# Kernel tuning notes

Hardware: AMD Instinct MI355X
Metric: run time of the kernel (lower is better)

The kernel has to match this reference:

```python
import jax, jax.numpy as jnp
import numpy as np

H = 8
SPLIT = 1
# deterministic stand-in for random.shuffle(range(8)) in the original
_PERM = np.random.RandomState(0).permutation(H)
SERIES_IDX = jnp.asarray(_PERM[SPLIT:])  # 7 heads
CROSS_IDX = jnp.asarray(_PERM[:SPLIT])   # 1 head


def setup_inputs() -> dict:
    key = jax.random.key(0)
    ks = jax.random.split(key, 5)
    B, L, E = 8, 1024, 64
    shp = (B, L, H, E)
    return {
        "queries": jax.random.normal(ks[0], shp, dtype=jnp.float32),
        "keys": jax.random.normal(ks[1], shp, dtype=jnp.float32),
        "keysT": jax.random.normal(ks[2], shp, dtype=jnp.float32),
        "values": jax.random.normal(ks[3], shp, dtype=jnp.float32),
        "valuesT": jax.random.normal(ks[4], shp, dtype=jnp.float32),
    }


def reference(queries, keys, keysT, values, valuesT):
    B, L, _, E = queries.shape
    scale = 1.0 / jnp.sqrt(jnp.asarray(E, dtype=queries.dtype))
    neg_inf = jnp.asarray(-jnp.inf, dtype=queries.dtype)

    # head split (gather along head dim)
    sq = queries[:, :, SERIES_IDX]   # [B,L,7,E]
    sk = keys[:, :, SERIES_IDX]      # [B,S,7,E]
    sv = values[:, :, SERIES_IDX]    # [B,S,7,D]
    cq = queries[:, :, CROSS_IDX]    # [B,L,1,E]
    ckT = keysT[:, :, CROSS_IDX]     # [B,C,1,E]
    cvT = valuesT[:, :, CROSS_IDX]   # [B,C,1,D]

    # causal mask: True above the diagonal -> disallowed
    causal = jnp.triu(jnp.ones((L, L), dtype=bool), k=1)  # [L,L]

    # series branch
    scores = jnp.einsum('blne,bsne->bnls', sq, sk)  # [B,7,L,S]
    scores = jnp.where(causal[None, None], neg_inf, scores * scale)
    series = jax.nn.softmax(scores, axis=-1)
    V = jnp.einsum('bhls,bshd->blhd', series, sv)   # [B,L,7,D]

    # cross branch
    cscores = jnp.einsum('blme,bcme->bmlc', cq, ckT)  # [B,1,L,C]
    cscores = jnp.where(causal[None, None], neg_inf, cscores * scale)
    crosses = jax.nn.softmax(cscores, axis=-1)
    V_cross = jnp.einsum('bhlc,bchd->blhd', crosses, cvT)  # [B,L,1,D]

    return jnp.concatenate([V, V_cross], axis=2)  # [B,L,8,D]
```

## Files before the change

kernel.cpp:

```cpp
#include <hip/hip_runtime.h>
#include <math.h>

#define Lq 1024
#define Hq 8
#define Eq 64
#define LDW 72

#define SRC_HEAD_PACKED 0x64503712u

typedef __bf16 bf16_t;
typedef __bf16 bf16x8 __attribute__((ext_vector_type(8)));
typedef __bf16 bf16x4 __attribute__((ext_vector_type(4)));
typedef float floatx4 __attribute__((ext_vector_type(4)));

__device__ __forceinline__ bf16x8 cvt8(const float4 a, const float4 b) {
    bf16x8 r;
    r[0] = (bf16_t)a.x; r[1] = (bf16_t)a.y; r[2] = (bf16_t)a.z; r[3] = (bf16_t)a.w;
    r[4] = (bf16_t)b.x; r[5] = (bf16_t)b.y; r[6] = (bf16_t)b.z; r[7] = (bf16_t)b.w;
    return r;
}

__global__ __launch_bounds__(256, 2)
void attn_mfma(const float* __restrict__ Q, const float* __restrict__ Ks,
               const float* __restrict__ KTs, const float* __restrict__ Vs,
               const float* __restrict__ VTs, float* __restrict__ out) {
    const int p    = blockIdx.x;
    const int slot = blockIdx.y;
    const int b    = blockIdx.z;
    const int h    = (SRC_HEAD_PACKED >> (slot * 4)) & 0xF;
    const float* __restrict__ Kp = (slot == 7) ? KTs : Ks;
    const float* __restrict__ Vp = (slot == 7) ? VTs : Vs;
    const int pA = p, pB = 15 - p;

    const int tid  = threadIdx.x;
    const int wv   = tid >> 6;
    const int lane = tid & 63;
    const int ln16 = lane & 15;
    const int quad = lane >> 4;

    __shared__ alignas(16) unsigned short k_lds[64][LDW];
    __shared__ alignas(16) unsigned short vt_lds[64][LDW];
    __shared__ alignas(16) unsigned short pt_lds[4][16][LDW];

    const float qs = 0.125f * 1.44269504f;
    bf16x8 qfA[2], qfB[2];
    {
        const int rA = pA * 64 + wv * 16 + ln16;
        const int rB = pB * 64 + wv * 16 + ln16;
        const float* qa = Q + (((size_t)b * Lq + rA) * Hq + h) * Eq + quad * 8;
        const float* qb = Q + (((size_t)b * Lq + rB) * Hq + h) * Eq + quad * 8;
        #pragma unroll
        for (int ec = 0; ec < 2; ++ec) {
            float4 f0 = ((const float4*)(qa + ec * 32))[0];
            float4 f1 = ((const float4*)(qa + ec * 32))[1];
            float4 g0 = ((const float4*)(qb + ec * 32))[0];
            float4 g1 = ((const float4*)(qb + ec * 32))[1];
            f0.x*=qs; f0.y*=qs; f0.z*=qs; f0.w*=qs; f1.x*=qs; f1.y*=qs; f1.z*=qs; f1.w*=qs;
            g0.x*=qs; g0.y*=qs; g0.z*=qs; g0.w*=qs; g1.x*=qs; g1.y*=qs; g1.z*=qs; g1.w*=qs;
            qfA[ec] = cvt8(f0, f1);
            qfB[ec] = cvt8(g0, g1);
        }
    }

    floatx4 OA[4], OB[4];
    #pragma unroll
    for (int i = 0; i < 4; ++i) { OA[i] = (floatx4){0,0,0,0}; OB[i] = (floatx4){0,0,0,0}; }
    float mA = -INFINITY, lA = 0.f, mB = -INFINITY, lB = 0.f;

    float4 kq[4];
    float  vq[16];
    const int kj = tid >> 2, kc = (tid & 3) * 16;
    const int vd = tid & 63, vk = (tid >> 6) * 16;

    auto load_tile = [&](int kt) {
        const float* kb = Kp + (((size_t)b * Lq + kt * 64 + kj) * Hq + h) * Eq + kc;
        kq[0] = ((const float4*)kb)[0]; kq[1] = ((const float4*)kb)[1];
        kq[2] = ((const float4*)kb)[2]; kq[3] = ((const float4*)kb)[3];
        const float* vb = Vp + (((size_t)b * Lq + kt * 64 + vk) * Hq + h) * Eq + vd;
        #pragma unroll
        for (int i = 0; i < 16; ++i) vq[i] = vb[(size_t)i * (Hq * Eq)];
    };

    auto process = [&](const bf16x8* qf, bf16x8 kf[4][2], bf16x8 vf[4][2],
                       floatx4* O, float& m, float& l, bool diag) {
        floatx4 s[4];
        #pragma unroll
        for (int nc = 0; nc < 4; ++nc) {
            floatx4 acc = (floatx4){0,0,0,0};
            acc = __builtin_amdgcn_mfma_f32_16x16x32_bf16(kf[nc][0], qf[0], acc, 0, 0, 0);
            acc = __builtin_amdgcn_mfma_f32_16x16x32_bf16(kf[nc][1], qf[1], acc, 0, 0, 0);
            s[nc] = acc;
        }
        if (diag) {
            const int rin = wv * 16 + ln16;
            #pragma unroll
            for (int nc = 0; nc < 4; ++nc)
                #pragma unroll
                for (int r = 0; r < 4; ++r)
                    if (nc * 16 + quad * 4 + r > rin) s[nc][r] = -INFINITY;
        }
        float mn = s[0][0];
        #pragma unroll
        for (int nc = 0; nc < 4; ++nc)
            #pragma unroll
            for (int r = 0; r < 4; ++r) mn = fmaxf(mn, s[nc][r]);
        mn = fmaxf(mn, __shfl_xor(mn, 16, 64));
        mn = fmaxf(mn, __shfl_xor(mn, 32, 64));
        mn = fmaxf(mn, m);
        const float alpha = __builtin_amdgcn_exp2f(m - mn);
        m = mn;
        float ps = 0.f;
        float pv[4][4];
        #pragma unroll
        for (int nc = 0; nc < 4; ++nc)
            #pragma unroll
            for (int r = 0; r < 4; ++r) { pv[nc][r] = __builtin_amdgcn_exp2f(s[nc][r] - mn); ps += pv[nc][r]; }
        ps += __shfl_xor(ps, 16, 64);
        ps += __shfl_xor(ps, 32, 64);
        l = l * alpha + ps;
        #pragma unroll
        for (int dc = 0; dc < 4; ++dc) O[dc] *= alpha;
        #pragma unroll
        for (int nc = 0; nc < 4; ++nc) {
            bf16x4 pk;
            pk[0] = (bf16_t)pv[nc][0]; pk[1] = (bf16_t)pv[nc][1];
            pk[2] = (bf16_t)pv[nc][2]; pk[3] = (bf16_t)pv[nc][3];
            *(bf16x4*)&pt_lds[wv][ln16][nc * 16 + quad * 4] = pk;
        }
        bf16x8 pf0 = *(const bf16x8*)&pt_lds[wv][ln16][quad * 8];
        bf16x8 pf1 = *(const bf16x8*)&pt_lds[wv][ln16][32 + quad * 8];
        #pragma unroll
        for (int dc = 0; dc < 4; ++dc) {
            O[dc] = __builtin_amdgcn_mfma_f32_16x16x32_bf16(vf[dc][0], pf0, O[dc], 0, 0, 0);
            O[dc] = __builtin_amdgcn_mfma_f32_16x16x32_bf16(vf[dc][1], pf1, O[dc], 0, 0, 0);
        }
    };

    load_tile(0);
    for (int kt = 0; kt <= pB; ++kt) {
        __syncthreads();
        *(bf16x8*)&k_lds[kj][kc]      = cvt8(kq[0], kq[1]);
        *(bf16x8*)&k_lds[kj][kc + 8]  = cvt8(kq[2], kq[3]);
        {
            const float4* vq4 = (const float4*)vq;
            *(bf16x8*)&vt_lds[vd][vk]     = cvt8(vq4[0], vq4[1]);
            *(bf16x8*)&vt_lds[vd][vk + 8] = cvt8(vq4[2], vq4[3]);
        }
        if (kt < pB) load_tile(kt + 1);
        __syncthreads();

        bf16x8 kf[4][2], vf[4][2];
        #pragma unroll
        for (int c = 0; c < 4; ++c) {
            kf[c][0] = *(const bf16x8*)&k_lds[c * 16 + ln16][quad * 8];
            kf[c][1] = *(const bf16x8*)&k_lds[c * 16 + ln16][32 + quad * 8];
            vf[c][0] = *(const bf16x8*)&vt_lds[c * 16 + ln16][quad * 8];
            vf[c][1] = *(const bf16x8*)&vt_lds[c * 16 + ln16][32 + quad * 8];
        }
        if (kt <= pA) process(qfA, kf, vf, OA, mA, lA, kt == pA);
        process(qfB, kf, vf, OB, mB, lB, kt == pB);
    }

    {
        const float inv = 1.0f / lA;
        const int row = pA * 64 + wv * 16 + ln16;
        float* op = out + (((size_t)b * Lq + row) * Hq + slot) * Eq + quad * 4;
        #pragma unroll
        for (int dc = 0; dc < 4; ++dc) {
            float4 o; o.x = OA[dc][0] * inv; o.y = OA[dc][1] * inv;
            o.z = OA[dc][2] * inv; o.w = OA[dc][3] * inv;
            *(float4*)(op + dc * 16) = o;
        }
    }
    {
        const float inv = 1.0f / lB;
        const int row = pB * 64 + wv * 16 + ln16;
        float* op = out + (((size_t)b * Lq + row) * Hq + slot) * Eq + quad * 4;
        #pragma unroll
        for (int dc = 0; dc < 4; ++dc) {
            float4 o; o.x = OB[dc][0] * inv; o.y = OB[dc][1] * inv;
            o.z = OB[dc][2] * inv; o.w = OB[dc][3] * inv;
            *(float4*)(op + dc * 16) = o;
        }
    }
}

extern "C" void kernel_launch(void* const* d_in, const int* in_sizes, int n_in,
                              void* d_out, int out_size, void* d_ws, size_t ws_size,
                              hipStream_t stream) {
    const float* queries = (const float*)d_in[0];
    const float* keys    = (const float*)d_in[1];
    const float* keysT   = (const float*)d_in[2];
    const float* values  = (const float*)d_in[3];
    const float* valuesT = (const float*)d_in[4];
    float* out = (float*)d_out;

    dim3 grid(8, Hq, 8);
    dim3 block(256);
    attn_mfma<<<grid, block, 0, stream>>>(queries, keys, keysT, values, valuesT, out);
}
```

Before: 143.9 us.

## Split each key tile across two wave groups with final softmax merge

Doubles the block to 512 threads (8 waves): each set of 4 waves handles half of each 64-key tile, keeping separate online-softmax states that are merged through shared memory at the end. This halves the per-wave MFMA and softmax work per tile, giving more waves to hide latency on a grid of only 512 blocks. The grid order is also changed so slot and batch vary fastest. In exchange it adds the LDS merge with extra barriers and more register and LDS pressure per block. Initial max is set to a finite value so a fully masked half does not produce NaN.

```diff
diff --git a/kernel.cpp b/kernel.cpp
--- a/kernel.cpp
+++ b/kernel.cpp
@@ -5,6 +5,7 @@
 #define Hq 8
 #define Eq 64
 #define LDW 72
+#define PTW 40
 
 #define SRC_HEAD_PACKED 0x64503712u
 
@@ -20,13 +21,13 @@
     return r;
 }
 
-__global__ __launch_bounds__(256, 2)
+__global__ __launch_bounds__(512, 4)
 void attn_mfma(const float* __restrict__ Q, const float* __restrict__ Ks,
                const float* __restrict__ KTs, const float* __restrict__ Vs,
                const float* __restrict__ VTs, float* __restrict__ out) {
-    const int p    = blockIdx.x;
-    const int slot = blockIdx.y;
-    const int b    = blockIdx.z;
+    const int slot = blockIdx.x;
+    const int b    = blockIdx.y;
+    const int p    = blockIdx.z;
     const int h    = (SRC_HEAD_PACKED >> (slot * 4)) & 0xF;
     const float* __restrict__ Kp = (slot == 7) ? KTs : Ks;
     const float* __restrict__ Vp = (slot == 7) ? VTs : Vs;
@@ -37,16 +38,19 @@
     const int lane = tid & 63;
     const int ln16 = lane & 15;
     const int quad = lane >> 4;
-
-    __shared__ alignas(16) unsigned short k_lds[64][LDW];
-    __shared__ alignas(16) unsigned short vt_lds[64][LDW];
-    __shared__ alignas(16) unsigned short pt_lds[4][16][LDW];
+    const int wq   = wv & 3;
+    const int kh   = wv >> 2;
+
+    __shared__ alignas(16) unsigned short smem[64 * LDW * 2 + 8 * 16 * PTW];
+    unsigned short (*k_lds)[LDW]  = (unsigned short (*)[LDW])smem;
+    unsigned short (*vt_lds)[LDW] = (unsigned short (*)[LDW])(smem + 64 * LDW);
+    unsigned short (*pt)[PTW]     = (unsigned short (*)[PTW])(smem + 2 * 64 * LDW + wv * 16 * PTW);
 
     const float qs = 0.125f * 1.44269504f;
     bf16x8 qfA[2], qfB[2];
     {
-        const int rA = pA * 64 + wv * 16 + ln16;
-        const int rB = pB * 64 + wv * 16 + ln16;
+        const int rA = pA * 64 + wq * 16 + ln16;
+        const int rB = pB * 64 + wq * 16 + ln16;
         const float* qa = Q + (((size_t)b * Lq + rA) * Hq + h) * Eq + quad * 8;
         const float* qb = Q + (((size_t)b * Lq + rB) * Hq + h) * Eq + quad * 8;
         #pragma unroll
@@ -65,43 +69,42 @@
     floatx4 OA[4], OB[4];
     #pragma unroll
     for (int i = 0; i < 4; ++i) { OA[i] = (floatx4){0,0,0,0}; OB[i] = (floatx4){0,0,0,0}; }
-    float mA = -INFINITY, lA = 0.f, mB = -INFINITY, lB = 0.f;
-
-    float4 kq[4];
-    float  vq[16];
-    const int kj = tid >> 2, kc = (tid & 3) * 16;
-    const int vd = tid & 63, vk = (tid >> 6) * 16;
+    float mA = -1e30f, lA = 0.f, mB = -1e30f, lB = 0.f;
+
+    float4 kq[2];
+    float  vq[8];
+    const int kj = tid >> 3, kc = (tid & 7) * 8;
+    const int vd = tid & 63, vk = wv * 8;
 
     auto load_tile = [&](int kt) {
         const float* kb = Kp + (((size_t)b * Lq + kt * 64 + kj) * Hq + h) * Eq + kc;
         kq[0] = ((const float4*)kb)[0]; kq[1] = ((const float4*)kb)[1];
-        kq[2] = ((const float4*)kb)[2]; kq[3] = ((const float4*)kb)[3];
         const float* vb = Vp + (((size_t)b * Lq + kt * 64 + vk) * Hq + h) * Eq + vd;
         #pragma unroll
-        for (int i = 0; i < 16; ++i) vq[i] = vb[(size_t)i * (Hq * Eq)];
+        for (int i = 0; i < 8; ++i) vq[i] = vb[(size_t)i * (Hq * Eq)];
     };
 
-    auto process = [&](const bf16x8* qf, bf16x8 kf[4][2], bf16x8 vf[4][2],
+    auto process = [&](const bf16x8* qf, const bf16x8 kf[2][2], const bf16x8 vf[4],
                        floatx4* O, float& m, float& l, bool diag) {
-        floatx4 s[4];
-        #pragma unroll
-        for (int nc = 0; nc < 4; ++nc) {
+        floatx4 s[2];
+        #pragma unroll
+        for (int nc = 0; nc < 2; ++nc) {
             floatx4 acc = (floatx4){0,0,0,0};
             acc = __builtin_amdgcn_mfma_f32_16x16x32_bf16(kf[nc][0], qf[0], acc, 0, 0, 0);
             acc = __builtin_amdgcn_mfma_f32_16x16x32_bf16(kf[nc][1], qf[1], acc, 0, 0, 0);
             s[nc] = acc;
         }
         if (diag) {
-            const int rin = wv * 16 + ln16;
+            const int rin = wq * 16 + ln16;
             #pragma unroll
-            for (int nc = 0; nc < 4; ++nc)
+            for (int nc = 0; nc < 2; ++nc)
                 #pragma unroll
                 for (int r = 0; r < 4; ++r)
-                    if (nc * 16 + quad * 4 + r > rin) s[nc][r] = -INFINITY;
+                    if (kh * 32 + nc * 16 + quad * 4 + r > rin) s[nc][r] = -INFINITY;
         }
         float mn = s[0][0];
         #pragma unroll
-        for (int nc = 0; nc < 4; ++nc)
+        for (int nc = 0; nc < 2; ++nc)
             #pragma unroll
             for (int r = 0; r < 4; ++r) mn = fmaxf(mn, s[nc][r]);
         mn = fmaxf(mn, __shfl_xor(mn, 16, 64));
@@ -110,9 +113,9 @@
         const float alpha = __builtin_amdgcn_exp2f(m - mn);
         m = mn;
         float ps = 0.f;
-        float pv[4][4];
-        #pragma unroll
-        for (int nc = 0; nc < 4; ++nc)
+        float pv[2][4];
+        #pragma unroll
+        for (int nc = 0; nc < 2; ++nc)
             #pragma unroll
             for (int r = 0; r < 4; ++r) { pv[nc][r] = __builtin_amdgcn_exp2f(s[nc][r] - mn); ps += pv[nc][r]; }
         ps += __shfl_xor(ps, 16, 64);
@@ -121,65 +124,103 @@
         #pragma unroll
         for (int dc = 0; dc < 4; ++dc) O[dc] *= alpha;
         #pragma unroll
-        for (int nc = 0; nc < 4; ++nc) {
+        for (int nc = 0; nc < 2; ++nc) {
             bf16x4 pk;
             pk[0] = (bf16_t)pv[nc][0]; pk[1] = (bf16_t)pv[nc][1];
             pk[2] = (bf16_t)pv[nc][2]; pk[3] = (bf16_t)pv[nc][3];
-            *(bf16x4*)&pt_lds[wv][ln16][nc * 16 + quad * 4] = pk;
-        }
-        bf16x8 pf0 = *(const bf16x8*)&pt_lds[wv][ln16][quad * 8];
-        bf16x8 pf1 = *(const bf16x8*)&pt_lds[wv][ln16][32 + quad * 8];
-        #pragma unroll
-        for (int dc = 0; dc < 4; ++dc) {
-            O[dc] = __builtin_amdgcn_mfma_f32_16x16x32_bf16(vf[dc][0], pf0, O[dc], 0, 0, 0);
-            O[dc] = __builtin_amdgcn_mfma_f32_16x16x32_bf16(vf[dc][1], pf1, O[dc], 0, 0, 0);
-        }
+            *(bf16x4*)&pt[ln16][nc * 16 + quad * 4] = pk;
+        }
+        bf16x8 pf = *(const bf16x8*)&pt[ln16][quad * 8];
+        #pragma unroll
+        for (int dc = 0; dc < 4; ++dc)
+            O[dc] = __builtin_amdgcn_mfma_f32_16x16x32_bf16(vf[dc], pf, O[dc], 0, 0, 0);
     };
 
     load_tile(0);
     for (int kt = 0; kt <= pB; ++kt) {
         __syncthreads();
-        *(bf16x8*)&k_lds[kj][kc]      = cvt8(kq[0], kq[1]);
-        *(bf16x8*)&k_lds[kj][kc + 8]  = cvt8(kq[2], kq[3]);
+        *(bf16x8*)&k_lds[kj][kc] = cvt8(kq[0], kq[1]);
         {
             const float4* vq4 = (const float4*)vq;
-            *(bf16x8*)&vt_lds[vd][vk]     = cvt8(vq4[0], vq4[1]);
-            *(bf16x8*)&vt_lds[vd][vk + 8] = cvt8(vq4[2], vq4[3]);
+            *(bf16x8*)&vt_lds[vd][vk] = cvt8(vq4[0], vq4[1]);
         }
         if (kt < pB) load_tile(kt + 1);
         __syncthreads();
 
-        bf16x8 kf[4][2], vf[4][2];
-        #pragma unroll
-        for (int c = 0; c < 4; ++c) {
-            kf[c][0] = *(const bf16x8*)&k_lds[c * 16 + ln16][quad * 8];
-            kf[c][1] = *(const bf16x8*)&k_lds[c * 16 + ln16][32 + quad * 8];
-            vf[c][0] = *(const bf16x8*)&vt_lds[c * 16 + ln16][quad * 8];
-            vf[c][1] = *(const bf16x8*)&vt_lds[c * 16 + ln16][32 + quad * 8];
-        }
+        bf16x8 kf[2][2], vf[4];
+        #pragma unroll
+        for (int c = 0; c < 2; ++c) {
+            kf[c][0] = *(const bf16x8*)&k_lds[(kh * 2 + c) * 16 + ln16][quad * 8];
+            kf[c][1] = *(const bf16x8*)&k_lds[(kh * 2 + c) * 16 + ln16][32 + quad * 8];
+        }
+        #pragma unroll
+        for (int c = 0; c < 4; ++c)
+            vf[c] = *(const bf16x8*)&vt_lds[c * 16 + ln16][kh * 32 + quad * 8];
+
         if (kt <= pA) process(qfA, kf, vf, OA, mA, lA, kt == pA);
         process(qfB, kf, vf, OB, mB, lB, kt == pB);
     }
 
-    {
-        const float inv = 1.0f / lA;
-        const int row = pA * 64 + wv * 16 + ln16;
+    __syncthreads();
+    float* mbuf = (float*)smem;
+
+    if (kh) {
+        float* dst = mbuf + (wq * 64 + lane) * 18;
+        #pragma unroll
+        for (int dc = 0; dc < 4; ++dc) {
+            *(float2*)(dst + dc * 4)     = make_float2(OA[dc][0], OA[dc][1]);
+            *(float2*)(dst + dc * 4 + 2) = make_float2(OA[dc][2], OA[dc][3]);
+        }
+        dst[16] = mA; dst[17] = lA;
+    }
+    __syncthreads();
+    if (!kh) {
+        const float* src = mbuf + (wq * 64 + lane) * 18;
+        const float m1 = src[16], l1 = src[17];
+        const float mm = fmaxf(mA, m1);
+        const float a0 = __builtin_amdgcn_exp2f(mA - mm);
+        const float a1 = __builtin_amdgcn_exp2f(m1 - mm);
+        const float inv = 1.0f / (lA * a0 + l1 * a1);
+        const int row = pA * 64 + wq * 16 + ln16;
         float* op = out + (((size_t)b * Lq + row) * Hq + slot) * Eq + quad * 4;
         #pragma unroll
         for (int dc = 0; dc < 4; ++dc) {
-            float4 o; o.x = OA[dc][0] * inv; o.y = OA[dc][1] * inv;
-            o.z = OA[dc][2] * inv; o.w = OA[dc][3] * inv;
+            float4 o;
+            o.x = (OA[dc][0] * a0 + src[dc * 4 + 0] * a1) * inv;
+            o.y = (OA[dc][1] * a0 + src[dc * 4 + 1] * a1) * inv;
+            o.z = (OA[dc][2] * a0 + src[dc * 4 + 2] * a1) * inv;
+            o.w = (OA[dc][3] * a0 + src[dc * 4 + 3] * a1) * inv;
             *(float4*)(op + dc * 16) = o;
         }
     }
-    {
-        const float inv = 1.0f / lB;
-        const int row = pB * 64 + wv * 16 + ln16;
+    __syncthreads();
+
+    if (kh) {
+        float* dst = mbuf + (wq * 64 + lane) * 18;
+        #pragma unroll
+        for (int dc = 0; dc < 4; ++dc) {
+            *(float2*)(dst + dc * 4)     = make_float2(OB[dc][0], OB[dc][1]);
+            *(float2*)(dst + dc * 4 + 2) = make_float2(OB[dc][2], OB[dc][3]);
+        }
+        dst[16] = mB; dst[17] = lB;
+    }
+    __syncthreads();
+    if (!kh) {
+        const float* src = mbuf + (wq * 64 + lane) * 18;
+        const float m1 = src[16], l1 = src[17];
+        const float mm = fmaxf(mB, m1);
+        const float a0 = __builtin_amdgcn_exp2f(mB - mm);
+        const float a1 = __builtin_amdgcn_exp2f(m1 - mm);
+        const float inv = 1.0f / (lB * a0 + l1 * a1);
+        const int row = pB * 64 + wq * 16 + ln16;
         float* op = out + (((size_t)b * Lq + row) * Hq + slot) * Eq + quad * 4;
         #pragma unroll
         for (int dc = 0; dc < 4; ++dc) {
-            float4 o; o.x = OB[dc][0] * inv; o.y = OB[dc][1] * inv;
-            o.z = OB[dc][2] * inv; o.w = OB[dc][3] * inv;
+            float4 o;
+            o.x = (OB[dc][0] * a0 + src[dc * 4 + 0] * a1) * inv;
+            o.y = (OB[dc][1] * a0 + src[dc * 4 + 1] * a1) * inv;
+            o.z = (OB[dc][2] * a0 + src[dc * 4 + 2] * a1) * inv;
+            o.w = (OB[dc][3] * a0 + src[dc * 4 + 3] * a1) * inv;
             *(float4*)(op + dc * 16) = o;
         }
     }
@@ -195,7 +236,7 @@
     const float* valuesT = (const float*)d_in[4];
     float* out = (float*)d_out;
 
-    dim3 grid(8, Hq, 8);
-    dim3 block(256);
+    dim3 grid(Hq, 8, 8);
+    dim3 block(512);
     attn_mfma<<<grid, block, 0, stream>>>(queries, keys, keysT, values, valuesT, out);
 }
```

Result: faster. 138.7 us (-3.6%).
